# Performance work log

Hardware: AMD Instinct MI355X
Metric: run time of the kernel (lower is better)

Reference implementation:

```python
import jax, jax.numpy as jnp
import numpy as np

N = 4096          # hypernodes
D = 256           # embedding_dim / hidden_dim
NUM_HEADS = 8
DEPTH = D // NUM_HEADS
N_LAYERS = 2
OUT_DIM = 4
M = N + 4         # hyperedges: N 'nebor' + 3 topo + 1 stroma
ALPHA = 0.5
LN_EPS = 1e-5


def setup_inputs() -> dict:
    key = jax.random.key(0)
    ks = jax.random.split(key, 32)
    X = jax.random.normal(ks[0], (N, D), dtype=jnp.float32)
    # sparse-ish binary incidence matrix; densify last 4 (topo/stroma) cols a bit
    H = (jax.random.uniform(ks[1], (N, M)) < 0.004).astype(jnp.float32)
    H = H.at[:, -4:].set((jax.random.uniform(ks[2], (N, 4)) < 0.5).astype(jnp.float32))
    # H2GT.forward: HIM[:, :-4] += diag(ones(N))
    H = H.at[:, :N].add(jnp.eye(N, dtype=jnp.float32))
    s = 0.02
    def lin(k, o, i):
        return jax.random.normal(k, (o, i), dtype=jnp.float32) * s
    inp = {"X": X, "H": H}
    # stacked per-HetHyper-layer params (torch nn.Linear convention: y = x @ W.T + b)
    names = ["Wq", "Wkn", "Wkt", "Wks", "fc"]
    for j, nm in enumerate(names):
        inp[nm + "_w"] = jax.random.normal(ks[3 + j], (N_LAYERS, D, D), dtype=jnp.float32) * s
        inp[nm + "_b"] = jnp.zeros((N_LAYERS, D), dtype=jnp.float32)
    inp["ln_g"] = jnp.ones((N_LAYERS, D), dtype=jnp.float32)
    inp["ln_b"] = jnp.zeros((N_LAYERS, D), dtype=jnp.float32)
    # Attn_Net_Gated (L=D, D=D, n_classes=1)
    inp["aw"] = lin(ks[10], D, D); inp["ab"] = jnp.zeros((D,), jnp.float32)
    inp["bw"] = lin(ks[11], D, D); inp["bb"] = jnp.zeros((D,), jnp.float32)
    inp["cw"] = lin(ks[12], 1, D); inp["cb"] = jnp.zeros((1,), jnp.float32)
    inp["out_w"] = lin(ks[13], OUT_DIM, D); inp["out_b"] = jnp.zeros((OUT_DIM,), jnp.float32)
    return inp


def _ln(x, g, b):
    m = jnp.mean(x, axis=-1, keepdims=True)
    v = jnp.mean(jnp.square(x - m), axis=-1, keepdims=True)
    return (x - m) * jax.lax.rsqrt(v + LN_EPS) * g + b


def _hethyper(X, H, Wq_w, Wq_b, Wkn_w, Wkn_b, Wkt_w, Wkt_b, Wks_w, Wks_b,
              fc_w, fc_b, ln_g, ln_b):
    # update_hyperedge: E = (H^T X) / deg
    deg = jnp.sum(H, axis=0)[:, None]                      # [M,1]
    E = (H.T @ X) / deg                                    # [M,D]
    Xn = _ln(X, ln_g, ln_b)
    En = _ln(E, ln_g, ln_b)
    q = (Xn @ Wq_w.T + Wq_b).reshape(-1, NUM_HEADS, DEPTH).transpose(1, 0, 2)  # [h,N,d]
    kn = En[:-4] @ Wkn_w.T + Wkn_b                          # [M-4,D]
    kt = En[-4:-1] @ Wkt_w.T + Wkt_b                        # [3,D]
    ks = En[-1:] @ Wks_w.T + Wks_b                          # [1,D]
    k = jnp.concatenate([kn, kt, ks], axis=0)
    k = k.reshape(-1, NUM_HEADS, DEPTH).transpose(1, 0, 2)  # [h,M,d]
    att = jnp.einsum('hnd,hmd->hnm', q, k) / (DEPTH ** 0.5)  # [h,N,M]
    att = jnp.where(H[None] == 0, -jnp.inf, att)
    att = jax.nn.softmax(att, axis=-1)                       # dropout is identity (eval)
    feat = jnp.einsum('hnm,hmd->hnd', att, k)                # [h,N,d]
    feat = feat.transpose(1, 0, 2).reshape(-1, NUM_HEADS * DEPTH)
    feat = jax.nn.relu(feat @ fc_w.T + fc_b)
    return feat * ALPHA + X * (1.0 - ALPHA)


def reference(X, H, Wq_w, Wq_b, Wkn_w, Wkn_b, Wkt_w, Wkt_b, Wks_w, Wks_b,
              fc_w, fc_b, ln_g, ln_b, aw, ab, bw, bb, cw, cb, out_w, out_b):
    feat = X
    for i in range(N_LAYERS):
        feat = _hethyper(feat, H, Wq_w[i], Wq_b[i], Wkn_w[i], Wkn_b[i],
                         Wkt_w[i], Wkt_b[i], Wks_w[i], Wks_b[i],
                         fc_w[i], fc_b[i], ln_g[i], ln_b[i])
    # Attn_Net_Gated
    a = jnp.tanh(feat @ aw.T + ab)
    b = jax.nn.sigmoid(feat @ bw.T + bb)
    A = (a * b) @ cw.T + cb                                  # [N,1]
    A = A.T                                                  # [1,N]
    pooled = jax.nn.softmax(A, axis=1) @ feat                # [1,D]
    return pooled @ out_w.T + out_b                          # [1,OUT_DIM]
```

## Files before the change

kernel.cpp:

```cpp
#include <hip/hip_runtime.h>
#include <math.h>

constexpr int kN = 4096;
constexpr int kM = 4100;
constexpr int kD = 256;
constexpr int ROWCAP = 64;
constexpr int COLCAP = 64;
constexpr int EB_CHUNKS = 64;
constexpr float kLnEps = 1e-5f;
constexpr float kScale = 0.17677669529663687f;

typedef short v8bf __attribute__((ext_vector_type(8)));
typedef float v4f  __attribute__((ext_vector_type(4)));

__device__ __forceinline__ float waveSum(float v) {
#pragma unroll
  for (int m = 32; m >= 1; m >>= 1) v += __shfl_xor(v, m);
  return v;
}
__device__ __forceinline__ float waveMax(float v) {
#pragma unroll
  for (int m = 32; m >= 1; m >>= 1) v = fmaxf(v, __shfl_xor(v, m));
  return v;
}
__device__ __forceinline__ float blockSum256(float v, float* sh) {
  v = waveSum(v);
  int lane = threadIdx.x & 63, w = threadIdx.x >> 6;
  __syncthreads();
  if (lane == 0) sh[w] = v;
  __syncthreads();
  return sh[0] + sh[1] + sh[2] + sh[3];
}

__device__ __forceinline__ short f2bf(float x) {
  unsigned u = __float_as_uint(x);
  unsigned r = (u + 0x7fffu + ((u >> 16) & 1u)) >> 16;
  return (short)r;
}
__device__ __forceinline__ float bf2f(short h) {
  return __uint_as_float(((unsigned)(unsigned short)h) << 16);
}
__device__ __forceinline__ int fragOff(int n, int k) {
  return ((n >> 4) << 12) + ((k >> 5) << 9) + (((k >> 3) & 3) << 7) + ((n & 15) << 3) + (k & 7);
}

struct WPtrs { const float* w[8]; };
__global__ __launch_bounds__(256) void k_wsplit(
    WPtrs wp, short* __restrict__ hi, short* __restrict__ lo,
    int* __restrict__ col_cnt) {
  int mat = blockIdx.y;
  int i = blockIdx.x * 256 + threadIdx.x;
  if (mat == 0 && blockIdx.x < 16) col_cnt[blockIdx.x * 256 + threadIdx.x] = 0;
  int out = i >> 8, k = i & 255;
  float v = wp.w[mat][i];
  short h = f2bf(v);
  size_t base = (size_t)mat * 65536 + fragOff(out, k);
  hi[base] = h;
  lo[base] = f2bf(v - bf2f(h));
}

__global__ __launch_bounds__(256) void k_build_csr(
    const float* __restrict__ H, int* __restrict__ row_cnt, int* __restrict__ row_idx,
    int* __restrict__ col_cnt, int* __restrict__ col_idx, float* __restrict__ col_val,
    float* __restrict__ Htail) {
  int n = (blockIdx.x * blockDim.x + threadIdx.x) >> 6;
  int lane = threadIdx.x & 63;
  const float* hrow = H + (size_t)n * kM;
  float4 v[16];
#pragma unroll
  for (int c = 0; c < 16; ++c) v[c] = *(const float4*)&hrow[c * 256 + lane * 4];
  float tv = (lane < 4) ? hrow[4096 + lane] : 0.0f;
  if (lane < 4) Htail[lane * kN + n] = tv;
  unsigned long long below = (1ull << lane) - 1ull;
  int cnt = 0;
#pragma unroll
  for (int c = 0; c < 16; ++c) {
    int mbase = c * 256 + lane * 4;
    float vv[4] = {v[c].x, v[c].y, v[c].z, v[c].w};
    unsigned long long bal[4];
#pragma unroll
    for (int j = 0; j < 4; ++j) bal[j] = __ballot(vv[j] != 0.0f);
    int pre = 0, tot = 0;
#pragma unroll
    for (int j = 0; j < 4; ++j) { pre += __popcll(bal[j] & below); tot += __popcll(bal[j]); }
    int local = 0;
#pragma unroll
    for (int j = 0; j < 4; ++j) {
      if (vv[j] != 0.0f) {
        int m = mbase + j;
        int pos = cnt + pre + local;
        if (pos < ROWCAP) row_idx[n * ROWCAP + pos] = m;
        int pc = atomicAdd(&col_cnt[m], 1);
        if (pc < COLCAP) { col_idx[m * COLCAP + pc] = n; col_val[m * COLCAP + pc] = vv[j]; }
        local++;
      }
    }
    cnt += tot;
  }
  unsigned long long bal = __ballot(tv != 0.0f);
  if (tv != 0.0f) {
    int pos = cnt + __popcll(bal & below);
    if (pos < ROWCAP) row_idx[n * ROWCAP + pos] = 4096 + lane;
  }
  cnt += __popcll(bal);
  if (lane == 0) row_cnt[n] = cnt < ROWCAP ? cnt : ROWCAP;
}

__global__ __launch_bounds__(256) void k_sort_csc(
    int* __restrict__ col_cnt, int* __restrict__ col_idx, float* __restrict__ col_val,
    float* __restrict__ deg) {
  int c = (blockIdx.x * blockDim.x + threadIdx.x) >> 6;
  int lane = threadIdx.x & 63;
  if (c < 4 && lane == 0) deg[kN + c] = 0.0f;
  int cnt = col_cnt[c]; if (cnt > COLCAP) cnt = COLCAP;
  int iv = 0x7fffffff; float vv = 0.0f;
  if (lane < cnt) { iv = col_idx[c * COLCAP + lane]; vv = col_val[c * COLCAP + lane]; }
  float dsum = waveSum(vv);
  int rank = 0;
  for (int j = 0; j < 64; ++j) {
    int ivj = __shfl(iv, j);
    if (ivj < iv) rank++;
  }
  if (lane < cnt) { col_idx[c * COLCAP + rank] = iv; col_val[c * COLCAP + rank] = vv; }
  if (lane == 0) { deg[c] = dsum; col_cnt[c] = cnt; }
}

__global__ __launch_bounds__(256) void k_pre(
    const float* __restrict__ X, const float* __restrict__ Htail,
    const int* __restrict__ col_cnt, const int* __restrict__ col_idx,
    const float* __restrict__ col_val, float* __restrict__ deg,
    const float* __restrict__ g, const float* __restrict__ b,
    short* __restrict__ Xnh, short* __restrict__ Xnl,
    short* __restrict__ Enh, short* __restrict__ Enl,
    float* __restrict__ ebpart, int add_deg) {
  __shared__ int sidx[4][COLCAP];
  __shared__ float sval[4][COLCAP];
  int bid = blockIdx.x, t = threadIdx.x;
  int wq = t >> 6, lane = t & 63;
  if (bid < 256) {
    __shared__ float hv[64];
    int c = bid >> 6, chunk = bid & 63;
    int r0 = chunk * 64;
    if (t < 64) {
      float hvv = Htail[c * kN + r0 + t];
      hv[t] = hvv;
      if (add_deg) {
        float ds = waveSum(hvv);
        if (t == 0 && ds != 0.0f) atomicAdd(&deg[kN + c], ds);
      }
    }
    __syncthreads();
    float s0 = 0.f, s1 = 0.f, s2 = 0.f, s3 = 0.f;
#pragma unroll
    for (int i = 0; i < 64; i += 4) {
      s0 += hv[i]     * X[(size_t)(r0 + i) * kD + t];
      s1 += hv[i + 1] * X[(size_t)(r0 + i + 1) * kD + t];
      s2 += hv[i + 2] * X[(size_t)(r0 + i + 2) * kD + t];
      s3 += hv[i + 3] * X[(size_t)(r0 + i + 3) * kD + t];
    }
    ebpart[(size_t)(c * EB_CHUNKS + chunk) * kD + t] = ((s0 + s1) + (s2 + s3));
  } else if (bid < 1280) {
    int m = (bid - 256) * 4 + wq;
    int cnt = col_cnt[m];
    if (lane < cnt) { sidx[wq][lane] = col_idx[m * COLCAP + lane]; sval[wq][lane] = col_val[m * COLCAP + lane]; }
    __syncthreads();
    float4 a0 = {0,0,0,0}, a1 = {0,0,0,0}, a2 = {0,0,0,0}, a3 = {0,0,0,0};
    int e = 0;
    for (; e + 3 < cnt; e += 4) {
      float v0 = sval[wq][e],     v1 = sval[wq][e + 1];
      float v2 = sval[wq][e + 2], v3 = sval[wq][e + 3];
      float4 x0 = *(const float4*)&X[(size_t)sidx[wq][e] * kD + lane * 4];
      float4 x1 = *(const float4*)&X[(size_t)sidx[wq][e + 1] * kD + lane * 4];
      float4 x2 = *(const float4*)&X[(size_t)sidx[wq][e + 2] * kD + lane * 4];
      float4 x3 = *(const float4*)&X[(size_t)sidx[wq][e + 3] * kD + lane * 4];
      a0.x += v0 * x0.x; a0.y += v0 * x0.y; a0.z += v0 * x0.z; a0.w += v0 * x0.w;
      a1.x += v1 * x1.x; a1.y += v1 * x1.y; a1.z += v1 * x1.z; a1.w += v1 * x1.w;
      a2.x += v2 * x2.x; a2.y += v2 * x2.y; a2.z += v2 * x2.z; a2.w += v2 * x2.w;
      a3.x += v3 * x3.x; a3.y += v3 * x3.y; a3.z += v3 * x3.z; a3.w += v3 * x3.w;
    }
    for (; e < cnt; ++e) {
      float v0 = sval[wq][e];
      float4 x0 = *(const float4*)&X[(size_t)sidx[wq][e] * kD + lane * 4];
      a0.x += v0 * x0.x; a0.y += v0 * x0.y; a0.z += v0 * x0.z; a0.w += v0 * x0.w;
    }
    float ax = (a0.x + a1.x) + (a2.x + a3.x);
    float ay = (a0.y + a1.y) + (a2.y + a3.y);
    float az = (a0.z + a1.z) + (a2.z + a3.z);
    float aw4 = (a0.w + a1.w) + (a2.w + a3.w);
    float inv = 1.0f / deg[m];
    ax *= inv; ay *= inv; az *= inv; aw4 *= inv;
    float mean = waveSum(ax + ay + az + aw4) * (1.0f / kD);
    float dx = ax - mean, dy = ay - mean, dz = az - mean, dw = aw4 - mean;
    float var = waveSum(dx * dx + dy * dy + dz * dz + dw * dw) * (1.0f / kD);
    float rstd = rsqrtf(var + kLnEps);
    float4 gv = *(const float4*)&g[lane * 4];
    float4 bv = *(const float4*)&b[lane * 4];
    float o0 = dx * rstd * gv.x + bv.x, o1 = dy * rstd * gv.y + bv.y;
    float o2 = dz * rstd * gv.z + bv.z, o3 = dw * rstd * gv.w + bv.w;
    int off = fragOff(m, lane * 4);
    short4 hi, lo;
    hi.x = f2bf(o0); lo.x = f2bf(o0 - bf2f(hi.x));
    hi.y = f2bf(o1); lo.y = f2bf(o1 - bf2f(hi.y));
    hi.z = f2bf(o2); lo.z = f2bf(o2 - bf2f(hi.z));
    hi.w = f2bf(o3); lo.w = f2bf(o3 - bf2f(hi.w));
    *(short4*)&Enh[off] = hi;
    *(short4*)&Enl[off] = lo;
  } else {
    int row = (bid - 1280) * 4 + wq;
    float4 v = *(const float4*)&X[(size_t)row * kD + lane * 4];
    float s = waveSum(v.x + v.y + v.z + v.w);
    float mean = s * (1.0f / kD);
    float dx = v.x - mean, dy = v.y - mean, dz = v.z - mean, dw = v.w - mean;
    float q = waveSum(dx * dx + dy * dy + dz * dz + dw * dw);
    float rstd = rsqrtf(q * (1.0f / kD) + kLnEps);
    float4 gv = *(const float4*)&g[lane * 4];
    float4 bv = *(const float4*)&b[lane * 4];
    float o0 = dx * rstd * gv.x + bv.x, o1 = dy * rstd * gv.y + bv.y;
    float o2 = dz * rstd * gv.z + bv.z, o3 = dw * rstd * gv.w + bv.w;
    int off = fragOff(row, lane * 4);
    short4 hi, lo;
    hi.x = f2bf(o0); lo.x = f2bf(o0 - bf2f(hi.x));
    hi.y = f2bf(o1); lo.y = f2bf(o1 - bf2f(hi.y));
    hi.z = f2bf(o2); lo.z = f2bf(o2 - bf2f(hi.z));
    hi.w = f2bf(o3); lo.w = f2bf(o3 - bf2f(hi.w));
    *(short4*)&Xnh[off] = hi;
    *(short4*)&Xnl[off] = lo;
  }
}

struct GArg {
  const short* Ah; const short* Al; const short* Wh; const short* Wl;
  const float* bias; float* C; const float* blend;
  short* Ch; short* Cl; int mode;
};
struct FArg {
  const float* part; const float* deg; const float* g; const float* b;
  const float* Wkt_w; const float* Wkt_b; const float* Wks_w; const float* Wks_b;
  float* K;
};

__global__ __launch_bounds__(256) void k_fgemm(GArg a0, GArg a1, FArg f) {
  int t = threadIdx.x;
  if (blockIdx.z == 2) {
    if (blockIdx.y != 0 || blockIdx.x >= 4) return;
    int c = blockIdx.x;
    __shared__ float er[kD];
    __shared__ float sh[4];
    float s0 = 0.f, s1 = 0.f, s2 = 0.f, s3 = 0.f;
    float s4 = 0.f, s5 = 0.f, s6 = 0.f, s7 = 0.f;
    const float* pp = f.part + (size_t)c * EB_CHUNKS * kD + t;
#pragma unroll
    for (int k = 0; k < EB_CHUNKS; k += 8) {
      s0 += pp[(k + 0) * kD]; s1 += pp[(k + 1) * kD];
      s2 += pp[(k + 2) * kD]; s3 += pp[(k + 3) * kD];
      s4 += pp[(k + 4) * kD]; s5 += pp[(k + 5) * kD];
      s6 += pp[(k + 6) * kD]; s7 += pp[(k + 7) * kD];
    }
    float s = (((s0 + s1) + (s2 + s3)) + ((s4 + s5) + (s6 + s7))) * (1.0f / f.deg[kN + c]);
    float mean = blockSum256(s, sh) * (1.0f / kD);
    float dv = s - mean;
    float var = blockSum256(dv * dv, sh) * (1.0f / kD);
    er[t] = dv * rsqrtf(var + kLnEps) * f.g[t] + f.b[t];
    __syncthreads();
    const float* W = (c < 3) ? f.Wkt_w : f.Wks_w;
    float acc = 0.f;
    for (int k = 0; k < kD; k += 4) {
      float4 wt = *(const float4*)&W[(size_t)t * kD + k];
      float4 e0 = *(const float4*)&er[k];
      acc += e0.x * wt.x + e0.y * wt.y + e0.z * wt.z + e0.w * wt.w;
    }
    float bt = (c < 3) ? f.Wkt_b[t] : f.Wks_b[t];
    f.K[(size_t)(kN + c) * kD + t] = acc + bt;
    return;
  }
  GArg ga = blockIdx.z ? a1 : a0;
  int wv = t >> 6, lane = t & 63;
  int l15 = lane & 15, sub = lane >> 4;
  int mt = blockIdx.x * 4 + wv;
  int ct0 = blockIdx.y * 4;
  const short* Ah = ga.Ah + mt * 4096;
  const short* Al = ga.Al + mt * 4096;
  v4f acc[4] = {{0,0,0,0},{0,0,0,0},{0,0,0,0},{0,0,0,0}};
#pragma unroll
  for (int kc = 0; kc < 8; ++kc) {
    v8bf ahi = *(const v8bf*)(Ah + kc * 512 + lane * 8);
    v8bf alo = *(const v8bf*)(Al + kc * 512 + lane * 8);
#pragma unroll
    for (int c = 0; c < 4; ++c) {
      int wo = (ct0 + c) * 4096 + kc * 512 + lane * 8;
      v8bf bhi = *(const v8bf*)(ga.Wh + wo);
      v8bf blo = *(const v8bf*)(ga.Wl + wo);
      acc[c] = __builtin_amdgcn_mfma_f32_16x16x32_bf16(ahi, bhi, acc[c], 0, 0, 0);
      acc[c] = __builtin_amdgcn_mfma_f32_16x16x32_bf16(alo, bhi, acc[c], 0, 0, 0);
      acc[c] = __builtin_amdgcn_mfma_f32_16x16x32_bf16(ahi, blo, acc[c], 0, 0, 0);
    }
  }
  int row0 = mt * 16, col0 = blockIdx.y * 64;
#pragma unroll
  for (int c = 0; c < 4; ++c) {
    int col = col0 + c * 16 + l15;
    float bs = ga.bias[col];
#pragma unroll
    for (int r = 0; r < 4; ++r) {
      int row = row0 + sub * 4 + r;
      float v = acc[c][r] + bs;
      if (ga.mode == 1) {
        float x0 = ga.blend[(size_t)row * kD + col];
        v = 0.5f * fmaxf(v, 0.0f) + 0.5f * x0;
      }
      ga.C[(size_t)row * kD + col] = v;
      if (ga.Ch) {
        int off = fragOff(row, col);
        short h = f2bf(v);
        ga.Ch[off] = h;
        ga.Cl[off] = f2bf(v - bf2f(h));
      }
    }
  }
}

__global__ __launch_bounds__(256) void k_fgemm_ab(
    const short* __restrict__ Ah, const short* __restrict__ Al,
    const short* __restrict__ Wah, const short* __restrict__ Wal,
    const float* __restrict__ ba,
    const short* __restrict__ Wbh, const short* __restrict__ Wbl,
    const float* __restrict__ bbv,
    const float* __restrict__ cw, float* __restrict__ gpart) {
  int t = threadIdx.x;
  int wv = t >> 6, lane = t & 63;
  int l15 = lane & 15, sub = lane >> 4;
  int mt = blockIdx.x * 4 + wv;
  int ct0 = blockIdx.y * 4;
  const short* Ahp = Ah + mt * 4096;
  const short* Alp = Al + mt * 4096;
  v4f acca[4] = {{0,0,0,0},{0,0,0,0},{0,0,0,0},{0,0,0,0}};
  v4f accb[4] = {{0,0,0,0},{0,0,0,0},{0,0,0,0},{0,0,0,0}};
#pragma unroll
  for (int kc = 0; kc < 8; ++kc) {
    v8bf ahi = *(const v8bf*)(Ahp + kc * 512 + lane * 8);
    v8bf alo = *(const v8bf*)(Alp + kc * 512 + lane * 8);
#pragma unroll
    for (int c = 0; c < 4; ++c) {
      int wo = (ct0 + c) * 4096 + kc * 512 + lane * 8;
      v8bf wah = *(const v8bf*)(Wah + wo);
      v8bf wal = *(const v8bf*)(Wal + wo);
      acca[c] = __builtin_amdgcn_mfma_f32_16x16x32_bf16(ahi, wah, acca[c], 0, 0, 0);
      acca[c] = __builtin_amdgcn_mfma_f32_16x16x32_bf16(alo, wah, acca[c], 0, 0, 0);
      acca[c] = __builtin_amdgcn_mfma_f32_16x16x32_bf16(ahi, wal, acca[c], 0, 0, 0);
      v8bf wbh = *(const v8bf*)(Wbh + wo);
      v8bf wbl = *(const v8bf*)(Wbl + wo);
      accb[c] = __builtin_amdgcn_mfma_f32_16x16x32_bf16(ahi, wbh, accb[c], 0, 0, 0);
      accb[c] = __builtin_amdgcn_mfma_f32_16x16x32_bf16(alo, wbh, accb[c], 0, 0, 0);
      accb[c] = __builtin_amdgcn_mfma_f32_16x16x32_bf16(ahi, wbl, accb[c], 0, 0, 0);
    }
  }
  int row0 = mt * 16, col0 = blockIdx.y * 64;
  float rs[4] = {0.f, 0.f, 0.f, 0.f};
#pragma unroll
  for (int c = 0; c < 4; ++c) {
    int col = col0 + c * 16 + l15;
    float bac = ba[col], bbc = bbv[col], cwc = cw[col];
#pragma unroll
    for (int r = 0; r < 4; ++r) {
      float a = tanhf(acca[c][r] + bac);
      float b = 1.0f / (1.0f + __expf(-(accb[c][r] + bbc)));
      rs[r] += a * b * cwc;
    }
  }
#pragma unroll
  for (int r = 0; r < 4; ++r) {
    rs[r] += __shfl_xor(rs[r], 1);
    rs[r] += __shfl_xor(rs[r], 2);
    rs[r] += __shfl_xor(rs[r], 4);
    rs[r] += __shfl_xor(rs[r], 8);
  }
  if (l15 == 0) {
#pragma unroll
    for (int r = 0; r < 4; ++r)
      gpart[(size_t)blockIdx.y * kN + row0 + sub * 4 + r] = rs[r];
  }
}

__global__ __launch_bounds__(256) void k_attn(
    const float* __restrict__ q, const float* __restrict__ kbuf,
    const int* __restrict__ row_cnt, const int* __restrict__ row_idx,
    short* __restrict__ fAh, short* __restrict__ fAl) {
  __shared__ int sm[ROWCAP];
  __shared__ float qls[kD];
  __shared__ float pls[8][ROWCAP];
  int n = blockIdx.x, t = threadIdx.x;
  int cnt = row_cnt[n];
  if (t < cnt) sm[t] = row_idx[n * ROWCAP + t];
  qls[t] = q[(size_t)n * kD + t];
  __syncthreads();
  int h = t >> 5, j = t & 31;
  float4 qv[8];
#pragma unroll
  for (int d4 = 0; d4 < 8; ++d4) qv[d4] = *(const float4*)&qls[h * 32 + d4 * 4];
  float s1 = 0.f, s2 = 0.f;
  if (j < cnt) {
    const float* kr = &kbuf[(size_t)sm[j] * kD + h * 32];
#pragma unroll
    for (int d4 = 0; d4 < 8; ++d4) {
      float4 kv = *(const float4*)&kr[d4 * 4];
      s1 += qv[d4].x * kv.x + qv[d4].y * kv.y + qv[d4].z * kv.z + qv[d4].w * kv.w;
    }
  }
  if (j + 32 < cnt) {
    const float* kr = &kbuf[(size_t)sm[j + 32] * kD + h * 32];
#pragma unroll
    for (int d4 = 0; d4 < 8; ++d4) {
      float4 kv = *(const float4*)&kr[d4 * 4];
      s2 += qv[d4].x * kv.x + qv[d4].y * kv.y + qv[d4].z * kv.z + qv[d4].w * kv.w;
    }
  }
  s1 *= kScale; s2 *= kScale;
  float v1 = (j < cnt) ? s1 : -3.4e38f;
  float v2 = (j + 32 < cnt) ? s2 : -3.4e38f;
  float mx = fmaxf(v1, v2);
#pragma unroll
  for (int mm = 16; mm >= 1; mm >>= 1) mx = fmaxf(mx, __shfl_xor(mx, mm));
  float p1 = (j < cnt) ? __expf(s1 - mx) : 0.0f;
  float p2 = (j + 32 < cnt) ? __expf(s2 - mx) : 0.0f;
  float ssum = p1 + p2;
#pragma unroll
  for (int mm = 16; mm >= 1; mm >>= 1) ssum += __shfl_xor(ssum, mm);
  float inv = 1.0f / ssum;
  pls[h][j] = p1 * inv;
  pls[h][j + 32] = p2 * inv;
  __syncthreads();
  const float* kb = kbuf + t;
  float ac0 = 0.f, ac1 = 0.f, ac2 = 0.f, ac3 = 0.f;
  int e = 0;
  for (; e + 3 < cnt; e += 4) {
    ac0 += pls[h][e]     * kb[(size_t)sm[e] * kD];
    ac1 += pls[h][e + 1] * kb[(size_t)sm[e + 1] * kD];
    ac2 += pls[h][e + 2] * kb[(size_t)sm[e + 2] * kD];
    ac3 += pls[h][e + 3] * kb[(size_t)sm[e + 3] * kD];
  }
  for (; e < cnt; ++e) ac0 += pls[h][e] * kb[(size_t)sm[e] * kD];
  float v = (ac0 + ac1) + (ac2 + ac3);
  int off = fragOff(n, t);
  short hh = f2bf(v);
  fAh[off] = hh;
  fAl[off] = f2bf(v - bf2f(hh));
}

__global__ __launch_bounds__(256) void k_pool_part(
    const float* __restrict__ gpart, const float* __restrict__ cb,
    const float* __restrict__ feat, float* __restrict__ part) {
  __shared__ float sh[4];
  int b = blockIdx.x, t = threadIdx.x;
  float cb0 = cb[0];
  float mx = -3.4e38f;
  for (int i = t; i < kN; i += 256) {
    float a = gpart[i] + gpart[kN + i] + gpart[2 * kN + i] + gpart[3 * kN + i] + cb0;
    mx = fmaxf(mx, a);
  }
  mx = waveMax(mx);
  int lane = t & 63, w = t >> 6;
  __syncthreads();
  if (lane == 0) sh[w] = mx;
  __syncthreads();
  mx = fmaxf(fmaxf(sh[0], sh[1]), fmaxf(sh[2], sh[3]));
  __syncthreads();
  float s = 0.0f;
  for (int i = t; i < kN; i += 256) {
    float a = gpart[i] + gpart[kN + i] + gpart[2 * kN + i] + gpart[3 * kN + i] + cb0;
    s += expf(a - mx);
  }
  s = blockSum256(s, sh);
  float inv = 1.0f / s;
  float acc = 0.0f;
  for (int r = 0; r < 64; ++r) {
    int n = b * 64 + r;
    float a = gpart[n] + gpart[kN + n] + gpart[2 * kN + n] + gpart[3 * kN + n] + cb0;
    float p = expf(a - mx) * inv;
    acc += p * feat[(size_t)n * kD + t];
  }
  part[(size_t)b * kD + t] = acc;
}

__global__ __launch_bounds__(256) void k_pool_fin(
    const float* __restrict__ part, const float* __restrict__ out_w,
    const float* __restrict__ out_b, float* __restrict__ out) {
  __shared__ float pooled[kD];
  int d = threadIdx.x;
  float s = 0.0f;
#pragma unroll
  for (int b = 0; b < 64; ++b) s += part[(size_t)b * kD + d];
  pooled[d] = s;
  __syncthreads();
  if (d < 4) {
    float o = out_b[d];
    for (int i = 0; i < kD; ++i) o += pooled[i] * out_w[(size_t)d * kD + i];
    out[d] = o;
  }
}

extern "C" void kernel_launch(void* const* d_in, const int* in_sizes, int n_in,
                              void* d_out, int out_size, void* d_ws, size_t ws_size,
                              hipStream_t stream) {
  (void)in_sizes; (void)n_in; (void)out_size; (void)ws_size;
  const float* X     = (const float*)d_in[0];
  const float* H     = (const float*)d_in[1];
  const float* Wq_w  = (const float*)d_in[2];
  const float* Wq_b  = (const float*)d_in[3];
  const float* Wkn_w = (const float*)d_in[4];
  const float* Wkn_b = (const float*)d_in[5];
  const float* Wkt_w = (const float*)d_in[6];
  const float* Wkt_b = (const float*)d_in[7];
  const float* Wks_w = (const float*)d_in[8];
  const float* Wks_b = (const float*)d_in[9];
  const float* fc_w  = (const float*)d_in[10];
  const float* fc_b  = (const float*)d_in[11];
  const float* ln_g  = (const float*)d_in[12];
  const float* ln_b  = (const float*)d_in[13];
  const float* aw    = (const float*)d_in[14];
  const float* ab    = (const float*)d_in[15];
  const float* bw    = (const float*)d_in[16];
  const float* bb    = (const float*)d_in[17];
  const float* cw    = (const float*)d_in[18];
  const float* cb    = (const float*)d_in[19];
  const float* out_w = (const float*)d_in[20];
  const float* out_b = (const float*)d_in[21];

  char* p = (char*)d_ws;
  auto alloc = [&](size_t bytes) -> void* {
    void* r = (void*)p;
    p += (bytes + 255) & ~(size_t)255;
    return r;
  };
  int*   row_cnt = (int*)alloc(kN * 4);
  int*   row_idx = (int*)alloc((size_t)kN * ROWCAP * 4);
  int*   col_cnt = (int*)alloc(kN * 4);
  int*   col_idx = (int*)alloc((size_t)kN * COLCAP * 4);
  float* col_val = (float*)alloc((size_t)kN * COLCAP * 4);
  float* Htail   = (float*)alloc((size_t)4 * kN * 4);
  float* deg     = (float*)alloc(kM * 4);
  float* qbuf    = (float*)alloc((size_t)kN * kD * 4);
  float* kbuf    = (float*)alloc((size_t)kM * kD * 4);
  float* buf0    = (float*)alloc((size_t)kN * kD * 4);
  float* buf1    = (float*)alloc((size_t)kN * kD * 4);
  float* ebpart  = (float*)alloc((size_t)4 * EB_CHUNKS * kD * 4);
  float* gpart   = (float*)alloc((size_t)4 * kN * 4);
  float* ppart   = (float*)alloc(64 * kD * 4);
  short* whi     = (short*)alloc((size_t)8 * 65536 * 2);
  short* wlo     = (short*)alloc((size_t)8 * 65536 * 2);
  short* Xnh     = (short*)alloc((size_t)kN * kD * 2);
  short* Xnl     = (short*)alloc((size_t)kN * kD * 2);
  short* Enh     = (short*)alloc((size_t)kN * kD * 2);
  short* Enl     = (short*)alloc((size_t)kN * kD * 2);
  short* fAh     = (short*)alloc((size_t)kN * kD * 2);
  short* fAl     = (short*)alloc((size_t)kN * kD * 2);
  short* b1h     = (short*)alloc((size_t)kN * kD * 2);
  short* b1l     = (short*)alloc((size_t)kN * kD * 2);

  WPtrs wp = {{Wq_w, Wq_w + 65536, Wkn_w, Wkn_w + 65536, fc_w, fc_w + 65536, aw, bw}};
  k_wsplit<<<dim3(256, 8), 256, 0, stream>>>(wp, whi, wlo, col_cnt);
  k_build_csr<<<kN / 4, 256, 0, stream>>>(H, row_cnt, row_idx, col_cnt, col_idx, col_val, Htail);
  k_sort_csc<<<kN / 4, 256, 0, stream>>>(col_cnt, col_idx, col_val, deg);

  FArg fdummy = {};
  GArg gdummy = {};
  for (int layer = 0; layer < 2; ++layer) {
    const float* Xc = layer ? buf0 : X;
    float* Xout = layer ? buf1 : buf0;
    size_t bo = (size_t)layer * kD;
    k_pre<<<2304, 256, 0, stream>>>(Xc, Htail, col_cnt, col_idx, col_val, deg,
                                    ln_g + bo, ln_b + bo, Xnh, Xnl, Enh, Enl,
                                    ebpart, layer == 0);
    GArg qa = {Xnh, Xnl, whi + (size_t)(0 + layer) * 65536, wlo + (size_t)(0 + layer) * 65536,
               Wq_b + bo, qbuf, nullptr, nullptr, nullptr, 0};
    GArg ka = {Enh, Enl, whi + (size_t)(2 + layer) * 65536, wlo + (size_t)(2 + layer) * 65536,
               Wkn_b + bo, kbuf, nullptr, nullptr, nullptr, 0};
    FArg fk = {ebpart, deg, ln_g + bo, ln_b + bo,
               Wkt_w + (size_t)layer * kD * kD, Wkt_b + bo,
               Wks_w + (size_t)layer * kD * kD, Wks_b + bo, kbuf};
    k_fgemm<<<dim3(64, 4, 3), 256, 0, stream>>>(qa, ka, fk);
    k_attn<<<kN, 256, 0, stream>>>(qbuf, kbuf, row_cnt, row_idx, fAh, fAl);
    GArg fa = {fAh, fAl, whi + (size_t)(4 + layer) * 65536, wlo + (size_t)(4 + layer) * 65536,
               fc_b + bo, Xout, Xc, layer ? b1h : nullptr, layer ? b1l : nullptr, 1};
    k_fgemm<<<dim3(64, 4, 1), 256, 0, stream>>>(fa, gdummy, fdummy);
  }

  k_fgemm_ab<<<dim3(64, 4), 256, 0, stream>>>(
      b1h, b1l, whi + (size_t)6 * 65536, wlo + (size_t)6 * 65536, ab,
      whi + (size_t)7 * 65536, wlo + (size_t)7 * 65536, bb, cw, gpart);
  k_pool_part<<<64, 256, 0, stream>>>(gpart, cb, buf1, ppart);
  k_pool_fin<<<1, 256, 0, stream>>>(ppart, out_w, out_b, (float*)d_out);
}
```

Baseline: 216.4 us.

## Fold CSC sort into k_pre, use deg partials, fuse pool finalize via last-block atomic

```diff
diff --git a/kernel.cpp b/kernel.cpp
--- a/kernel.cpp
+++ b/kernel.cpp
@@ -47,10 +47,11 @@
 struct WPtrs { const float* w[8]; };
 __global__ __launch_bounds__(256) void k_wsplit(
     WPtrs wp, short* __restrict__ hi, short* __restrict__ lo,
-    int* __restrict__ col_cnt) {
+    int* __restrict__ col_cnt, int* __restrict__ done) {
   int mat = blockIdx.y;
   int i = blockIdx.x * 256 + threadIdx.x;
   if (mat == 0 && blockIdx.x < 16) col_cnt[blockIdx.x * 256 + threadIdx.x] = 0;
+  if (mat == 0 && blockIdx.x == 16 && threadIdx.x == 0) *done = 0;
   int out = i >> 8, k = i & 255;
   float v = wp.w[mat][i];
   short h = f2bf(v);
@@ -106,33 +107,14 @@
   if (lane == 0) row_cnt[n] = cnt < ROWCAP ? cnt : ROWCAP;
 }
 
-__global__ __launch_bounds__(256) void k_sort_csc(
-    int* __restrict__ col_cnt, int* __restrict__ col_idx, float* __restrict__ col_val,
-    float* __restrict__ deg) {
-  int c = (blockIdx.x * blockDim.x + threadIdx.x) >> 6;
-  int lane = threadIdx.x & 63;
-  if (c < 4 && lane == 0) deg[kN + c] = 0.0f;
-  int cnt = col_cnt[c]; if (cnt > COLCAP) cnt = COLCAP;
-  int iv = 0x7fffffff; float vv = 0.0f;
-  if (lane < cnt) { iv = col_idx[c * COLCAP + lane]; vv = col_val[c * COLCAP + lane]; }
-  float dsum = waveSum(vv);
-  int rank = 0;
-  for (int j = 0; j < 64; ++j) {
-    int ivj = __shfl(iv, j);
-    if (ivj < iv) rank++;
-  }
-  if (lane < cnt) { col_idx[c * COLCAP + rank] = iv; col_val[c * COLCAP + rank] = vv; }
-  if (lane == 0) { deg[c] = dsum; col_cnt[c] = cnt; }
-}
-
 __global__ __launch_bounds__(256) void k_pre(
     const float* __restrict__ X, const float* __restrict__ Htail,
     const int* __restrict__ col_cnt, const int* __restrict__ col_idx,
-    const float* __restrict__ col_val, float* __restrict__ deg,
+    const float* __restrict__ col_val,
     const float* __restrict__ g, const float* __restrict__ b,
     short* __restrict__ Xnh, short* __restrict__ Xnl,
     short* __restrict__ Enh, short* __restrict__ Enl,
-    float* __restrict__ ebpart, int add_deg) {
+    float* __restrict__ ebpart, float* __restrict__ deg_part) {
   __shared__ int sidx[4][COLCAP];
   __shared__ float sval[4][COLCAP];
   int bid = blockIdx.x, t = threadIdx.x;
@@ -144,10 +126,8 @@
     if (t < 64) {
       float hvv = Htail[c * kN + r0 + t];
       hv[t] = hvv;
-      if (add_deg) {
-        float ds = waveSum(hvv);
-        if (t == 0 && ds != 0.0f) atomicAdd(&deg[kN + c], ds);
-      }
+      float ds = waveSum(hvv);
+      if (t == 0) deg_part[c * 64 + chunk] = ds;
     }
     __syncthreads();
     float s0 = 0.f, s1 = 0.f, s2 = 0.f, s3 = 0.f;
@@ -161,8 +141,16 @@
     ebpart[(size_t)(c * EB_CHUNKS + chunk) * kD + t] = ((s0 + s1) + (s2 + s3));
   } else if (bid < 1280) {
     int m = (bid - 256) * 4 + wq;
-    int cnt = col_cnt[m];
-    if (lane < cnt) { sidx[wq][lane] = col_idx[m * COLCAP + lane]; sval[wq][lane] = col_val[m * COLCAP + lane]; }
+    int cnt = col_cnt[m]; if (cnt > COLCAP) cnt = COLCAP;
+    int iv = 0x7fffffff; float vvl = 0.0f;
+    if (lane < cnt) { iv = col_idx[m * COLCAP + lane]; vvl = col_val[m * COLCAP + lane]; }
+    float dsum = waveSum(vvl);
+    int rank = 0;
+    for (int j = 0; j < 64; ++j) {
+      int ivj = __shfl(iv, j);
+      if (ivj < iv) rank++;
+    }
+    if (lane < cnt) { sidx[wq][rank] = iv; sval[wq][rank] = vvl; }
     __syncthreads();
     float4 a0 = {0,0,0,0}, a1 = {0,0,0,0}, a2 = {0,0,0,0}, a3 = {0,0,0,0};
     int e = 0;
@@ -187,7 +175,7 @@
     float ay = (a0.y + a1.y) + (a2.y + a3.y);
     float az = (a0.z + a1.z) + (a2.z + a3.z);
     float aw4 = (a0.w + a1.w) + (a2.w + a3.w);
-    float inv = 1.0f / deg[m];
+    float inv = 1.0f / dsum;
     ax *= inv; ay *= inv; az *= inv; aw4 *= inv;
     float mean = waveSum(ax + ay + az + aw4) * (1.0f / kD);
     float dx = ax - mean, dy = ay - mean, dz = az - mean, dw = aw4 - mean;
@@ -234,7 +222,7 @@
   short* Ch; short* Cl; int mode;
 };
 struct FArg {
-  const float* part; const float* deg; const float* g; const float* b;
+  const float* part; const float* deg_part; const float* g; const float* b;
   const float* Wkt_w; const float* Wkt_b; const float* Wks_w; const float* Wks_b;
   float* K;
 };
@@ -246,6 +234,10 @@
     int c = blockIdx.x;
     __shared__ float er[kD];
     __shared__ float sh[4];
+    float degsum = 0.f;
+    const float* dp = f.deg_part + c * 64;
+#pragma unroll
+    for (int k = 0; k < 64; ++k) degsum += dp[k];
     float s0 = 0.f, s1 = 0.f, s2 = 0.f, s3 = 0.f;
     float s4 = 0.f, s5 = 0.f, s6 = 0.f, s7 = 0.f;
     const float* pp = f.part + (size_t)c * EB_CHUNKS * kD + t;
@@ -256,7 +248,7 @@
       s4 += pp[(k + 4) * kD]; s5 += pp[(k + 5) * kD];
       s6 += pp[(k + 6) * kD]; s7 += pp[(k + 7) * kD];
     }
-    float s = (((s0 + s1) + (s2 + s3)) + ((s4 + s5) + (s6 + s7))) * (1.0f / f.deg[kN + c]);
+    float s = (((s0 + s1) + (s2 + s3)) + ((s4 + s5) + (s6 + s7))) * (1.0f / degsum);
     float mean = blockSum256(s, sh) * (1.0f / kD);
     float dv = s - mean;
     float var = blockSum256(dv * dv, sh) * (1.0f / kD);
@@ -446,10 +438,14 @@
   fAl[off] = f2bf(v - bf2f(hh));
 }
 
-__global__ __launch_bounds__(256) void k_pool_part(
+__global__ __launch_bounds__(256) void k_pool(
     const float* __restrict__ gpart, const float* __restrict__ cb,
-    const float* __restrict__ feat, float* __restrict__ part) {
+    const float* __restrict__ feat, float* __restrict__ part,
+    const float* __restrict__ out_w, const float* __restrict__ out_b,
+    float* __restrict__ out, int* __restrict__ done) {
   __shared__ float sh[4];
+  __shared__ float pooled[kD];
+  __shared__ int lastFlag;
   int b = blockIdx.x, t = threadIdx.x;
   float cb0 = cb[0];
   float mx = -3.4e38f;
@@ -479,22 +475,24 @@
     acc += p * feat[(size_t)n * kD + t];
   }
   part[(size_t)b * kD + t] = acc;
-}
-
-__global__ __launch_bounds__(256) void k_pool_fin(
-    const float* __restrict__ part, const float* __restrict__ out_w,
-    const float* __restrict__ out_b, float* __restrict__ out) {
-  __shared__ float pooled[kD];
-  int d = threadIdx.x;
-  float s = 0.0f;
-#pragma unroll
-  for (int b = 0; b < 64; ++b) s += part[(size_t)b * kD + d];
-  pooled[d] = s;
-  __syncthreads();
-  if (d < 4) {
-    float o = out_b[d];
-    for (int i = 0; i < kD; ++i) o += pooled[i] * out_w[(size_t)d * kD + i];
-    out[d] = o;
+  __threadfence();
+  if (t == 0) {
+    int old = atomicAdd(done, 1);
+    lastFlag = (old == 63) ? 1 : 0;
+  }
+  __syncthreads();
+  if (lastFlag) {
+    __threadfence();
+    float s2 = 0.0f;
+#pragma unroll
+    for (int q = 0; q < 64; ++q) s2 += part[(size_t)q * kD + t];
+    pooled[t] = s2;
+    __syncthreads();
+    if (t < 4) {
+      float o = out_b[t];
+      for (int i = 0; i < kD; ++i) o += pooled[i] * out_w[(size_t)t * kD + i];
+      out[t] = o;
+    }
   }
 }
 
@@ -531,35 +529,35 @@
     p += (bytes + 255) & ~(size_t)255;
     return r;
   };
-  int*   row_cnt = (int*)alloc(kN * 4);
-  int*   row_idx = (int*)alloc((size_t)kN * ROWCAP * 4);
-  int*   col_cnt = (int*)alloc(kN * 4);
-  int*   col_idx = (int*)alloc((size_t)kN * COLCAP * 4);
-  float* col_val = (float*)alloc((size_t)kN * COLCAP * 4);
-  float* Htail   = (float*)alloc((size_t)4 * kN * 4);
-  float* deg     = (float*)alloc(kM * 4);
-  float* qbuf    = (float*)alloc((size_t)kN * kD * 4);
-  float* kbuf    = (float*)alloc((size_t)kM * kD * 4);
-  float* buf0    = (float*)alloc((size_t)kN * kD * 4);
-  float* buf1    = (float*)alloc((size_t)kN * kD * 4);
-  float* ebpart  = (float*)alloc((size_t)4 * EB_CHUNKS * kD * 4);
-  float* gpart   = (float*)alloc((size_t)4 * kN * 4);
-  float* ppart   = (float*)alloc(64 * kD * 4);
-  short* whi     = (short*)alloc((size_t)8 * 65536 * 2);
-  short* wlo     = (short*)alloc((size_t)8 * 65536 * 2);
-  short* Xnh     = (short*)alloc((size_t)kN * kD * 2);
-  short* Xnl     = (short*)alloc((size_t)kN * kD * 2);
-  short* Enh     = (short*)alloc((size_t)kN * kD * 2);
-  short* Enl     = (short*)alloc((size_t)kN * kD * 2);
-  short* fAh     = (short*)alloc((size_t)kN * kD * 2);
-  short* fAl     = (short*)alloc((size_t)kN * kD * 2);
-  short* b1h     = (short*)alloc((size_t)kN * kD * 2);
-  short* b1l     = (short*)alloc((size_t)kN * kD * 2);
+  int*   row_cnt  = (int*)alloc(kN * 4);
+  int*   row_idx  = (int*)alloc((size_t)kN * ROWCAP * 4);
+  int*   col_cnt  = (int*)alloc(kN * 4);
+  int*   col_idx  = (int*)alloc((size_t)kN * COLCAP * 4);
+  float* col_val  = (float*)alloc((size_t)kN * COLCAP * 4);
+  float* Htail    = (float*)alloc((size_t)4 * kN * 4);
+  float* deg_part = (float*)alloc(4 * 64 * 4);
+  int*   done     = (int*)alloc(256);
+  float* qbuf     = (float*)alloc((size_t)kN * kD * 4);
+  float* kbuf     = (float*)alloc((size_t)kM * kD * 4);
+  float* buf0     = (float*)alloc((size_t)kN * kD * 4);
+  float* buf1     = (float*)alloc((size_t)kN * kD * 4);
+  float* ebpart   = (float*)alloc((size_t)4 * EB_CHUNKS * kD * 4);
+  float* gpart    = (float*)alloc((size_t)4 * kN * 4);
+  float* ppart    = (float*)alloc(64 * kD * 4);
+  short* whi      = (short*)alloc((size_t)8 * 65536 * 2);
+  short* wlo      = (short*)alloc((size_t)8 * 65536 * 2);
+  short* Xnh      = (short*)alloc((size_t)kN * kD * 2);
+  short* Xnl      = (short*)alloc((size_t)kN * kD * 2);
+  short* Enh      = (short*)alloc((size_t)kN * kD * 2);
+  short* Enl      = (short*)alloc((size_t)kN * kD * 2);
+  short* fAh      = (short*)alloc((size_t)kN * kD * 2);
+  short* fAl      = (short*)alloc((size_t)kN * kD * 2);
+  short* b1h      = (short*)alloc((size_t)kN * kD * 2);
+  short* b1l      = (short*)alloc((size_t)kN * kD * 2);
 
   WPtrs wp = {{Wq_w, Wq_w + 65536, Wkn_w, Wkn_w + 65536, fc_w, fc_w + 65536, aw, bw}};
-  k_wsplit<<<dim3(256, 8), 256, 0, stream>>>(wp, whi, wlo, col_cnt);
+  k_wsplit<<<dim3(256, 8), 256, 0, stream>>>(wp, whi, wlo, col_cnt, done);
   k_build_csr<<<kN / 4, 256, 0, stream>>>(H, row_cnt, row_idx, col_cnt, col_idx, col_val, Htail);
-  k_sort_csc<<<kN / 4, 256, 0, stream>>>(col_cnt, col_idx, col_val, deg);
 
   FArg fdummy = {};
   GArg gdummy = {};
@@ -567,14 +565,14 @@
     const float* Xc = layer ? buf0 : X;
     float* Xout = layer ? buf1 : buf0;
     size_t bo = (size_t)layer * kD;
-    k_pre<<<2304, 256, 0, stream>>>(Xc, Htail, col_cnt, col_idx, col_val, deg,
+    k_pre<<<2304, 256, 0, stream>>>(Xc, Htail, col_cnt, col_idx, col_val,
                                     ln_g + bo, ln_b + bo, Xnh, Xnl, Enh, Enl,
-                                    ebpart, layer == 0);
+                                    ebpart, deg_part);
     GArg qa = {Xnh, Xnl, whi + (size_t)(0 + layer) * 65536, wlo + (size_t)(0 + layer) * 65536,
                Wq_b + bo, qbuf, nullptr, nullptr, nullptr, 0};
     GArg ka = {Enh, Enl, whi + (size_t)(2 + layer) * 65536, wlo + (size_t)(2 + layer) * 65536,
                Wkn_b + bo, kbuf, nullptr, nullptr, nullptr, 0};
-    FArg fk = {ebpart, deg, ln_g + bo, ln_b + bo,
+    FArg fk = {ebpart, deg_part, ln_g + bo, ln_b + bo,
                Wkt_w + (size_t)layer * kD * kD, Wkt_b + bo,
                Wks_w + (size_t)layer * kD * kD, Wks_b + bo, kbuf};
     k_fgemm<<<dim3(64, 4, 3), 256, 0, stream>>>(qa, ka, fk);
@@ -587,6 +585,6 @@
   k_fgemm_ab<<<dim3(64, 4), 256, 0, stream>>>(
       b1h, b1l, whi + (size_t)6 * 65536, wlo + (size_t)6 * 65536, ab,
       whi + (size_t)7 * 65536, wlo + (size_t)7 * 65536, bb, cw, gpart);
-  k_pool_part<<<64, 256, 0, stream>>>(gpart, cb, buf1, ppart);
-  k_pool_fin<<<1, 256, 0, stream>>>(ppart, out_w, out_b, (float*)d_out);
-}
+  k_pool<<<64, 256, 0, stream>>>(gpart, cb, buf1, ppart, out_w, out_b,
+                                 (float*)d_out, done);
+}
```

Measured after the change: 215.5 us. Within noise of the previous version (-0.4%).
